# Performance work log

Hardware: AMD Instinct MI355X
Metric: run time of the kernel (lower is better)

Reference implementation:

```python
import jax, jax.numpy as jnp
import numpy as np

N, M = 4096, 2048
INPUT_SIZE = 128
QD = 32
IN_DIM = 2 * INPUT_SIZE + 1  # 257


def _gate(xg, q, W, b):
    # Fused weight-generation + apply: equivalent to
    # W1 = einsum('nd,dio->nio', q, W); out = bmm(xg[:,None,:], W1)[:,0,:] + q @ b
    return jnp.einsum('ni,nd,dio->no', xg, q, W) + q @ b


def setup_inputs() -> dict:
    key = jax.random.key(0)
    ks = jax.random.split(key, 12)
    xav_w = float(np.sqrt(6.0 / (IN_DIM + INPUT_SIZE)))
    xav_b = float(np.sqrt(6.0 / (QD + INPUT_SIZE)))
    mkW = lambda k: jax.random.uniform(k, (QD, IN_DIM, INPUT_SIZE), jnp.float32, -xav_w, xav_w)
    mkb = lambda k: jax.random.uniform(k, (QD, INPUT_SIZE), jnp.float32, -xav_b, xav_b)
    return {
        'x': jax.random.normal(ks[0], (N, INPUT_SIZE + 1), jnp.float32),
        'h': jax.random.normal(ks[1], (N, INPUT_SIZE), jnp.float32),
        'query_vectors': jax.random.normal(ks[2], (M, QD), jnp.float32),
        'adj': jax.random.uniform(ks[3], (N, N), jnp.float32) / N,  # row-normalized-ish
        'nodes_ind': jnp.arange(M, dtype=jnp.int32),
        'W_u': mkW(ks[4]), 'b_u': mkb(ks[5]),
        'W_r': mkW(ks[6]), 'b_r': mkb(ks[7]),
        'W_c': mkW(ks[8]), 'b_c': mkb(ks[9]),
    }


def reference(x, h, query_vectors, adj, nodes_ind, W_u, b_u, W_r, b_r, W_c, b_c):
    # graph convolution over concatenated [x, h] -> [N, 2*I+1]
    combined = adj @ jnp.concatenate([x, h], axis=-1)
    cg = combined[nodes_ind]  # [M, 257]
    r = jax.nn.sigmoid(_gate(cg, query_vectors, W_r, b_r))
    u = jax.nn.sigmoid(_gate(cg, query_vectors, W_u, b_u))
    h = h.at[nodes_ind].set(r * h[nodes_ind])
    cn = jnp.concatenate([x, h], axis=-1)[nodes_ind]  # [M, 257]
    cand = jnp.tanh(_gate(cn, query_vectors, W_c, b_c))
    new_h = (1.0 - u) * h[nodes_ind] + u * cand  # [M, 128]
    return new_h
```

## Files before the change

kernel.cpp:

```cpp
#include <hip/hip_runtime.h>
#include <hip/hip_bf16.h>

typedef unsigned short u16;
typedef unsigned int u32;
typedef __attribute__((ext_vector_type(8))) short bf16x8;
typedef __attribute__((ext_vector_type(4))) float f32x4;

#define NN 4096
#define MQ 2048
#define QDIM 32
#define IND 257
#define NSTEP 258
#define K2 (NSTEP*32)
#define HD 128
#define XD 129
#define CATP 320

__device__ __forceinline__ u16 f2bf(float f){
    u32 x = __float_as_uint(f);
    return (u16)((x + 0x7fffu + ((x>>16)&1u)) >> 16);
}

__device__ __forceinline__ void gload16(const void* g, void* l){
    __builtin_amdgcn_global_load_lds((const __attribute__((address_space(1))) unsigned int*)g,
                                     (__attribute__((address_space(3))) unsigned int*)l,
                                     16, 0, 0);
}

__device__ __forceinline__ bf16x8 lds_read8(const void* base, int byte_off){
    return *(const bf16x8*)((const char*)base + byte_off);
}

__device__ __forceinline__ bf16x8 mk_afrag(const float* q8, float f){
    union { bf16x8 v; __hip_bfloat162 h[4]; } u;
    #pragma unroll
    for (int p = 0; p < 4; ++p){
        float2 t; t.x = q8[2*p]*f; t.y = q8[2*p+1]*f;
        u.h[p] = __float22bfloat162_rn(t);
    }
    return u.v;
}

__global__ __launch_bounds__(128) void k_cvt_w2(const float* __restrict__ Wr,
                                                const float* __restrict__ Wu,
                                                const float* __restrict__ Wc,
                                                const float* __restrict__ br,
                                                const float* __restrict__ bu,
                                                const float* __restrict__ bc,
                                                u16* __restrict__ WT2ru,
                                                u16* __restrict__ WT2c){
    const int i = blockIdx.x, g = blockIdx.y, o = threadIdx.x;
    const float* W = (g==0)?Wr:(g==1)?Wu:Wc;
    const float* B = (g==0)?br:(g==1)?bu:bc;
    u16* dst = (g==0)? WT2ru + (size_t)o*K2
             : (g==1)? WT2ru + (size_t)(128+o)*K2
                     : WT2c  + (size_t)o*K2;
    alignas(16) u16 buf[32];
    if (i < IND){
        #pragma unroll
        for (int d = 0; d < 32; ++d) buf[d] = f2bf(W[((size_t)d*IND + i)*HD + o]);
    } else {
        #pragma unroll
        for (int d = 0; d < 32; ++d) buf[d] = f2bf(B[(size_t)d*HD + o]);
    }
    #pragma unroll
    for (int v = 0; v < 4; ++v)
        *reinterpret_cast<uint4*>(dst + i*32 + v*8) = *reinterpret_cast<const uint4*>(&buf[v*8]);
}

__global__ __launch_bounds__(256) void k_zero(float* __restrict__ p){
    reinterpret_cast<float4*>(p)[blockIdx.x*256 + threadIdx.x] = float4{0.f,0.f,0.f,0.f};
}

__global__ __launch_bounds__(256) void k_pack_catT(const float* __restrict__ x,
                                                   const float* __restrict__ h,
                                                   u16* __restrict__ catT){
    const int t = blockIdx.x*256 + threadIdx.x;
    const int c = blockIdx.y;
    const int k = t*8;
    alignas(16) u16 o[8];
    #pragma unroll
    for (int i = 0; i < 8; ++i){
        int node = k + i;
        float v = (c < XD) ? x[(size_t)node*XD + c]
                : (c < IND) ? h[(size_t)node*HD + (c - XD)] : 0.f;
        o[i] = f2bf(v);
    }
    *reinterpret_cast<uint4*>(catT + (size_t)c*NN + k) = *reinterpret_cast<const uint4*>(o);
}

__global__ __launch_bounds__(256) void k_conv_mfma(const float* __restrict__ adj,
                                                   const u16* __restrict__ catT,
                                                   const int* __restrict__ idx,
                                                   float* __restrict__ cg){
    __shared__ u16 Asm[64*64];
    __shared__ u16 Bsm[64*64];
    __shared__ int rows[64];
    const int tid = threadIdx.x;
    const int wave = tid >> 6, lane = tid & 63;
    const int m0 = blockIdx.y*64, n0 = blockIdx.x*64;
    const int s = blockIdx.z;
    if (tid < 64) rows[tid] = idx[m0 + tid];
    __syncthreads();

    const int trow = tid >> 2, kq = (tid & 3)*16;
    const float* arow = adj + (size_t)rows[trow]*NN;
    const int r7 = trow & 7;
    char* aw0 = (char*)Asm + trow*128 + (((kq*2)      ) ^ (r7<<4));
    char* aw1 = (char*)Asm + trow*128 + (((kq*2) + 16 ) ^ (r7<<4));

    const int sw = (((lane&7) ^ (lane>>3)) << 4);
    const char* pB = (const char*)catT + (size_t)(n0 + wave*16 + (lane>>3))*(NN*2) + sw;
    char* lB = (char*)Bsm + wave*2048;

    const int la = lane & 15, lh = lane >> 4;
    const int wr = wave >> 1, wc = wave & 1;
    f32x4 acc[2][2] = {};

    for (int k0 = s*512; k0 < s*512 + 512; k0 += 64){
        gload16(pB + (size_t)k0*2,                    lB);
        gload16(pB + (size_t)k0*2 + (size_t)8*(NN*2), lB + 1024);
        alignas(16) u16 tmp[16];
        #pragma unroll
        for (int v = 0; v < 4; ++v){
            float4 f = *reinterpret_cast<const float4*>(arow + k0 + kq + v*4);
            tmp[v*4+0] = f2bf(f.x); tmp[v*4+1] = f2bf(f.y);
            tmp[v*4+2] = f2bf(f.z); tmp[v*4+3] = f2bf(f.w);
        }
        *reinterpret_cast<uint4*>(aw0) = *reinterpret_cast<const uint4*>(&tmp[0]);
        *reinterpret_cast<uint4*>(aw1) = *reinterpret_cast<const uint4*>(&tmp[8]);
        __syncthreads();
        #pragma unroll
        for (int ks = 0; ks < 2; ++ks){
            const int kb = ks*64 + lh*16;
            bf16x8 a0 = lds_read8(Asm, (wr*32 +  0 + la)*128 + (kb ^ ((la&7)<<4)));
            bf16x8 a1 = lds_read8(Asm, (wr*32 + 16 + la)*128 + (kb ^ ((la&7)<<4)));
            bf16x8 b0 = lds_read8(Bsm, (wc*32 +  0 + la)*128 + (kb ^ ((la&7)<<4)));
            bf16x8 b1 = lds_read8(Bsm, (wc*32 + 16 + la)*128 + (kb ^ ((la&7)<<4)));
            acc[0][0] = __builtin_amdgcn_mfma_f32_16x16x32_bf16(a0, b0, acc[0][0], 0, 0, 0);
            acc[0][1] = __builtin_amdgcn_mfma_f32_16x16x32_bf16(a0, b1, acc[0][1], 0, 0, 0);
            acc[1][0] = __builtin_amdgcn_mfma_f32_16x16x32_bf16(a1, b0, acc[1][0], 0, 0, 0);
            acc[1][1] = __builtin_amdgcn_mfma_f32_16x16x32_bf16(a1, b1, acc[1][1], 0, 0, 0);
        }
        __syncthreads();
    }
    #pragma unroll
    for (int fr = 0; fr < 2; ++fr)
        #pragma unroll
        for (int fc = 0; fc < 2; ++fc){
            int m = m0 + wr*32 + fr*16 + lh*4;
            int n = n0 + wc*32 + fc*16 + la;
            #pragma unroll
            for (int j = 0; j < 4; ++j)
                atomicAdd(&cg[(size_t)(m+j)*CATP + n], acc[fr][fc][j]);
        }
}

__global__ __launch_bounds__(256) void k_gate_fused(const float* __restrict__ feat,
                                                    const float* __restrict__ q,
                                                    const u16* __restrict__ WT2,
                                                    float* __restrict__ S, int N){
    __shared__ float featLds[33*64];
    __shared__ u16 Bsm[64*32];
    const int tid = threadIdx.x;
    const int wave = tid >> 6, lane = tid & 63;
    const int la = lane & 15, lh = lane >> 4;
    const int m0 = blockIdx.y*64, n0 = blockIdx.x*64;
    const int z = blockIdx.z;
    const int i0 = z*32 + (z < 2 ? z : 2);
    const int cnt = (z < 2) ? 33 : 32;

    {
        const int row = tid >> 2, iq = tid & 3;
        #pragma unroll
        for (int j = 0; j < 9; ++j){
            int il = j*4 + iq;
            if (il < cnt){
                int gi = i0 + il;
                featLds[il*64 + row] = (gi == IND) ? 1.0f
                                     : feat[(size_t)(m0 + row)*CATP + gi];
            }
        }
    }
    const int wr = wave >> 1, wc = wave & 1;
    const int r0l = wr*32 + la, r1l = r0l + 16;
    const float* q0p = q + (size_t)(m0 + r0l)*QDIM + lh*8;
    const float* q1p = q + (size_t)(m0 + r1l)*QDIM + lh*8;
    float q80[8], q81[8];
    *reinterpret_cast<float4*>(&q80[0]) = *reinterpret_cast<const float4*>(q0p);
    *reinterpret_cast<float4*>(&q80[4]) = *reinterpret_cast<const float4*>(q0p + 4);
    *reinterpret_cast<float4*>(&q81[0]) = *reinterpret_cast<const float4*>(q1p);
    *reinterpret_cast<float4*>(&q81[4]) = *reinterpret_cast<const float4*>(q1p + 4);

    const int cc = tid >> 2;
    const int jj = (lane & 3) ^ ((cc >> 1) & 3);
    const u16* pB = WT2 + (size_t)(n0 + cc)*K2 + jj*8;
    char* lB = (char*)Bsm + wave*1024;

    const int col0 = wc*32 + la, col1 = col0 + 16;
    const int b0off = col0*64 + ((lh ^ ((col0>>1)&3)) << 4);
    const int b1off = col1*64 + ((lh ^ ((col1>>1)&3)) << 4);

    f32x4 acc[2][2] = {};
    __syncthreads();

    for (int s = 0; s < cnt; ++s){
        gload16(pB + (size_t)(i0 + s)*32, lB);
        __syncthreads();
        float f0 = featLds[s*64 + r0l];
        float f1 = featLds[s*64 + r1l];
        bf16x8 a0 = mk_afrag(q80, f0);
        bf16x8 a1 = mk_afrag(q81, f1);
        bf16x8 b0 = lds_read8(Bsm, b0off);
        bf16x8 b1 = lds_read8(Bsm, b1off);
        acc[0][0] = __builtin_amdgcn_mfma_f32_16x16x32_bf16(a0, b0, acc[0][0], 0, 0, 0);
        acc[0][1] = __builtin_amdgcn_mfma_f32_16x16x32_bf16(a0, b1, acc[0][1], 0, 0, 0);
        acc[1][0] = __builtin_amdgcn_mfma_f32_16x16x32_bf16(a1, b0, acc[1][0], 0, 0, 0);
        acc[1][1] = __builtin_amdgcn_mfma_f32_16x16x32_bf16(a1, b1, acc[1][1], 0, 0, 0);
        __syncthreads();
    }
    #pragma unroll
    for (int fr = 0; fr < 2; ++fr)
        #pragma unroll
        for (int fc = 0; fc < 2; ++fc){
            int m = m0 + wr*32 + fr*16 + lh*4;
            int n = n0 + wc*32 + fc*16 + la;
            #pragma unroll
            for (int j = 0; j < 4; ++j)
                atomicAdd(&S[(size_t)(m+j)*N + n], acc[fr][fc][j]);
        }
}

__global__ __launch_bounds__(256) void k_act1(const float* __restrict__ S1,
                                              const float* __restrict__ h,
                                              const float* __restrict__ x,
                                              const int* __restrict__ idx,
                                              float* __restrict__ featf2,
                                              float* __restrict__ u_ws){
    const int n = blockIdx.x, t = threadIdx.x;
    const int row = idx[n];
    if (t < HD){
        float rr = 1.f/(1.f + expf(-S1[(size_t)n*256 + t]));
        float uu = 1.f/(1.f + expf(-S1[(size_t)n*256 + 128 + t]));
        featf2[(size_t)n*CATP + XD + t] = rr * h[(size_t)row*HD + t];
        u_ws[(size_t)n*HD + t] = uu;
    }
    if (t < XD) featf2[(size_t)n*CATP + t] = x[(size_t)row*XD + t];
}

__global__ __launch_bounds__(256) void k_act2(const float* __restrict__ Sc,
                                              const float* __restrict__ featf2,
                                              const float* __restrict__ u_ws,
                                              float* __restrict__ out){
    int id = blockIdx.x*256 + threadIdx.x;
    int n = id >> 7, o = id & 127;
    float hupd = featf2[(size_t)n*CATP + XD + o];
    float uu = u_ws[id];
    out[id] = (1.f - uu)*hupd + uu*tanhf(Sc[id]);
}

extern "C" void kernel_launch(void* const* d_in, const int* in_sizes, int n_in,
                              void* d_out, int out_size, void* d_ws, size_t ws_size,
                              hipStream_t stream) {
    (void)in_sizes; (void)n_in; (void)out_size; (void)ws_size;
    const float* x   = (const float*)d_in[0];
    const float* h   = (const float*)d_in[1];
    const float* q   = (const float*)d_in[2];
    const float* adj = (const float*)d_in[3];
    const int*   idx = (const int*)d_in[4];
    const float* Wu  = (const float*)d_in[5];
    const float* bu  = (const float*)d_in[6];
    const float* Wr  = (const float*)d_in[7];
    const float* br  = (const float*)d_in[8];
    const float* Wc  = (const float*)d_in[9];
    const float* bc  = (const float*)d_in[10];
    float* out = (float*)d_out;

    char* wsb = (char*)d_ws;
    u16*   catT   = (u16*)  (wsb + 0);
    u16*   WT2ru  = (u16*)  (wsb + 2621440);
    u16*   WT2c   = (u16*)  (wsb + 6848512);
    float* cg     = (float*)(wsb + 8962048);
    float* S1     = (float*)(wsb + 11583488);
    float* Sc     = (float*)(wsb + 13680640);
    float* featf2 = (float*)(wsb + 14729216);
    float* u_ws   = (float*)(wsb + 17350656);

    k_cvt_w2    <<<dim3(NSTEP, 3),          128, 0, stream>>>(Wr, Wu, Wc, br, bu, bc, WT2ru, WT2c);
    k_zero      <<<dim3(1408),              256, 0, stream>>>(cg);
    k_pack_catT <<<dim3(2, CATP),           256, 0, stream>>>(x, h, catT);
    k_conv_mfma <<<dim3(CATP/64, MQ/64, 8), 256, 0, stream>>>(adj, catT, idx, cg);
    k_gate_fused<<<dim3(4, MQ/64, 8),       256, 0, stream>>>(cg, q, WT2ru, S1, 256);
    k_act1      <<<dim3(MQ),                256, 0, stream>>>(S1, h, x, idx, featf2, u_ws);
    k_gate_fused<<<dim3(2, MQ/64, 8),       256, 0, stream>>>(featf2, q, WT2c, Sc, 128);
    k_act2      <<<dim3(MQ*HD/256),         256, 0, stream>>>(Sc, featf2, u_ws, out);
}
```

Before: 222.5 us.

## Remap block indices for XCD locality and double-buffer gate weight loads

The conv and gate kernels switch to 1-D grids with a manual block-index remap. The remap is meant to place blocks that share adj rows or weight columns on the same XCD, so L2 reuse improves across the MI355X's chiplets. The gate kernel also double-buffers its LDS weight tile, issuing the next step's global-to-LDS load before computing the current one. Explicit vmcnt waits and raw s_barrier replace __syncthreads, which adds correctness risk around LDS hazards and buffer reuse.

```diff
diff --git a/kernel.cpp b/kernel.cpp
--- a/kernel.cpp
+++ b/kernel.cpp
@@ -96,10 +96,15 @@
     __shared__ u16 Asm[64*64];
     __shared__ u16 Bsm[64*64];
     __shared__ int rows[64];
+    const int b = blockIdx.x;
+    const int xcdr = b & 7, t = b >> 3;
+    const int xb = t % 5;
+    const int g  = (t / 5)*8 + xcdr;
+    const int yb = g & 31, s = g >> 5;
+    const int m0 = yb*64, n0 = xb*64;
+
     const int tid = threadIdx.x;
     const int wave = tid >> 6, lane = tid & 63;
-    const int m0 = blockIdx.y*64, n0 = blockIdx.x*64;
-    const int s = blockIdx.z;
     if (tid < 64) rows[tid] = idx[m0 + tid];
     __syncthreads();
 
@@ -156,19 +161,26 @@
         }
 }
 
+template<int LG>
 __global__ __launch_bounds__(256) void k_gate_fused(const float* __restrict__ feat,
                                                     const float* __restrict__ q,
                                                     const u16* __restrict__ WT2,
                                                     float* __restrict__ S, int N){
     __shared__ float featLds[33*64];
-    __shared__ u16 Bsm[64*32];
+    __shared__ u16 Bsm[2][64*32];
+    const int b = blockIdx.x;
+    const int xcdr = b & 7, t = b >> 3;
+    const int xb  = xcdr >> LG;
+    const int sub = xcdr & ((1<<LG)-1);
+    const int yb  = t & 31;
+    const int z   = ((t >> 5) << LG) | sub;
+    const int m0 = yb*64, n0 = xb*64;
+    const int i0 = z*32 + (z < 2 ? z : 2);
+    const int cnt = (z < 2) ? 33 : 32;
+
     const int tid = threadIdx.x;
     const int wave = tid >> 6, lane = tid & 63;
     const int la = lane & 15, lh = lane >> 4;
-    const int m0 = blockIdx.y*64, n0 = blockIdx.x*64;
-    const int z = blockIdx.z;
-    const int i0 = z*32 + (z < 2 ? z : 2);
-    const int cnt = (z < 2) ? 33 : 32;
 
     {
         const int row = tid >> 2, iq = tid & 3;
@@ -195,29 +207,41 @@
     const int cc = tid >> 2;
     const int jj = (lane & 3) ^ ((cc >> 1) & 3);
     const u16* pB = WT2 + (size_t)(n0 + cc)*K2 + jj*8;
-    char* lB = (char*)Bsm + wave*1024;
+    char* lB0 = (char*)&Bsm[0][0] + wave*1024;
+    char* lB1 = (char*)&Bsm[1][0] + wave*1024;
 
     const int col0 = wc*32 + la, col1 = col0 + 16;
     const int b0off = col0*64 + ((lh ^ ((col0>>1)&3)) << 4);
     const int b1off = col1*64 + ((lh ^ ((col1>>1)&3)) << 4);
 
     f32x4 acc[2][2] = {};
+
+    asm volatile("s_waitcnt vmcnt(0)" ::: "memory");
     __syncthreads();
+    gload16(pB + (size_t)i0*32, lB0);
 
     for (int s = 0; s < cnt; ++s){
-        gload16(pB + (size_t)(i0 + s)*32, lB);
-        __syncthreads();
+        if (s + 1 < cnt){
+            gload16(pB + (size_t)(i0 + s + 1)*32, (s & 1) ? lB0 : lB1);
+            asm volatile("s_waitcnt vmcnt(1)" ::: "memory");
+        } else {
+            asm volatile("s_waitcnt vmcnt(0)" ::: "memory");
+        }
+        __builtin_amdgcn_sched_barrier(0);
+        __builtin_amdgcn_s_barrier();
         float f0 = featLds[s*64 + r0l];
         float f1 = featLds[s*64 + r1l];
         bf16x8 a0 = mk_afrag(q80, f0);
         bf16x8 a1 = mk_afrag(q81, f1);
-        bf16x8 b0 = lds_read8(Bsm, b0off);
-        bf16x8 b1 = lds_read8(Bsm, b1off);
+        const char* base = (const char*)&Bsm[s & 1][0];
+        bf16x8 b0 = lds_read8(base, b0off);
+        bf16x8 b1 = lds_read8(base, b1off);
         acc[0][0] = __builtin_amdgcn_mfma_f32_16x16x32_bf16(a0, b0, acc[0][0], 0, 0, 0);
         acc[0][1] = __builtin_amdgcn_mfma_f32_16x16x32_bf16(a0, b1, acc[0][1], 0, 0, 0);
         acc[1][0] = __builtin_amdgcn_mfma_f32_16x16x32_bf16(a1, b0, acc[1][0], 0, 0, 0);
         acc[1][1] = __builtin_amdgcn_mfma_f32_16x16x32_bf16(a1, b1, acc[1][1], 0, 0, 0);
-        __syncthreads();
+        __builtin_amdgcn_s_barrier();
+        __builtin_amdgcn_sched_barrier(0);
     }
     #pragma unroll
     for (int fr = 0; fr < 2; ++fr)
@@ -286,12 +310,12 @@
     float* featf2 = (float*)(wsb + 14729216);
     float* u_ws   = (float*)(wsb + 17350656);
 
-    k_cvt_w2    <<<dim3(NSTEP, 3),          128, 0, stream>>>(Wr, Wu, Wc, br, bu, bc, WT2ru, WT2c);
-    k_zero      <<<dim3(1408),              256, 0, stream>>>(cg);
-    k_pack_catT <<<dim3(2, CATP),           256, 0, stream>>>(x, h, catT);
-    k_conv_mfma <<<dim3(CATP/64, MQ/64, 8), 256, 0, stream>>>(adj, catT, idx, cg);
-    k_gate_fused<<<dim3(4, MQ/64, 8),       256, 0, stream>>>(cg, q, WT2ru, S1, 256);
-    k_act1      <<<dim3(MQ),                256, 0, stream>>>(S1, h, x, idx, featf2, u_ws);
-    k_gate_fused<<<dim3(2, MQ/64, 8),       256, 0, stream>>>(featf2, q, WT2c, Sc, 128);
-    k_act2      <<<dim3(MQ*HD/256),         256, 0, stream>>>(Sc, featf2, u_ws, out);
-}
+    k_cvt_w2       <<<dim3(NSTEP, 3), 128, 0, stream>>>(Wr, Wu, Wc, br, bu, bc, WT2ru, WT2c);
+    k_zero         <<<dim3(1408),     256, 0, stream>>>(cg);
+    k_pack_catT    <<<dim3(2, CATP),  256, 0, stream>>>(x, h, catT);
+    k_conv_mfma    <<<dim3(1280),     256, 0, stream>>>(adj, catT, idx, cg);
+    k_gate_fused<1><<<dim3(1024),     256, 0, stream>>>(cg, q, WT2ru, S1, 256);
+    k_act1         <<<dim3(MQ),       256, 0, stream>>>(S1, h, x, idx, featf2, u_ws);
+    k_gate_fused<2><<<dim3(512),      256, 0, stream>>>(featf2, q, WT2c, Sc, 128);
+    k_act2         <<<dim3(MQ*HD/256),256, 0, stream>>>(Sc, featf2, u_ws, out);
+}
```

Result: faster. 210.2 us (-5.5%).
